# Optimization experiments

Hardware: AMD Instinct MI355X
Metric: run time of the kernel (lower is better)

The kernel has to match this reference:

```python
import jax, jax.numpy as jnp
import numpy as np

NH = 12      # config.n_head
LEVEL = 2    # config.level -> Lmin = 4


def setup_inputs() -> dict:
    key = jax.random.key(0)
    ks = jax.random.split(key, 10)
    B, T, C = 1, 2048, 768
    hs = C // NH
    s = 0.02
    return {
        'x':   jax.random.normal(ks[0], (B, T, C), jnp.float32),
        'Wq':  jax.random.normal(ks[1], (C, C), jnp.float32) * s,
        'Wk':  jax.random.normal(ks[2], (C, C), jnp.float32) * s,
        'Wv':  jax.random.normal(ks[3], (C, C), jnp.float32) * s,
        'Wks': jax.random.normal(ks[4], (hs * hs, hs), jnp.float32) * s,
        'bks': jax.random.normal(ks[5], (hs,), jnp.float32) * s,
        'Wvs': jax.random.normal(ks[6], (hs * hs, hs), jnp.float32) * s,
        'bvs': jax.random.normal(ks[7], (hs,), jnp.float32) * s,
        'Wc':  jax.random.normal(ks[8], (C, C), jnp.float32) * s,
        'bc':  jax.random.normal(ks[9], (C,), jnp.float32) * s,
    }


def reference(x, Wq, Wk, Wv, Wks, bks, Wvs, bvs, Wc, bc):
    B, T, C = x.shape
    hs = C // NH
    Lmin = 2 ** LEVEL
    levelmax = int(np.log2(T))          # T is a power of two -> no ragged tails per level
    scale = hs ** -0.5

    # fla LinearAttention preprocess: bias-free projections + elu feature map (phi = elu+1)
    q = (jax.nn.elu(x @ Wq) + 1.0).reshape(B, T, NH, hs)
    k = (jax.nn.elu(x @ Wk) + 1.0).reshape(B, T, NH, hs)
    v = (x @ Wv).reshape(B, T, NH, hs)

    # per-position linear-attn state increments phi(k) v^T  [B,T,H,hs,hs]
    kv = jnp.einsum('bthi,bthj->bthij', k, v).reshape(B, T, NH, hs * hs)

    # tail features: running state within each block of Lmin (fused_recurrent final states
    # over the ragged per-position tail segments [t - t%Lmin, t])
    tail_feat = jnp.cumsum(kv.reshape(B, T // Lmin, Lmin, NH, hs * hs), axis=2)
    tail_feat = tail_feat.reshape(B, T, NH, hs * hs)

    # hierarchical set features: dyadic block sums at levels LEVEL..levelmax
    cur = kv.reshape(B, T // Lmin, Lmin, NH, hs * hs).sum(axis=2)
    feats, ends = [], []
    for l in range(LEVEL, levelmax + 1):
        n = T // (2 ** l)
        feats.append(cur)
        ends.append(np.arange(1, n + 1) * (2 ** l))   # exclusive end index of each set
        if n >= 2:
            cur = cur.reshape(B, n // 2, 2, NH, hs * hs).sum(axis=2)
    set_feat = jnp.concatenate(feats, axis=1)          # [B, S, H, hs*hs], S = 1023
    ends = np.concatenate(ends)                        # [S]
    mask = ends[None, :] <= (np.arange(T) + 1)[:, None]  # [T, S] causal set mask

    # k_mapping / v_mapping: Linear(hs^2 -> hs)
    K = set_feat @ Wks + bks        # [B,S,H,hs]
    V = set_feat @ Wvs + bvs
    K_tail = tail_feat @ Wks + bks  # [B,T,H,hs]
    V_tail = tail_feat @ Wvs + bvs

    logits = jnp.einsum('bthd,bshd->bhts', q, K) * scale      # [B,H,T,S]
    logits = jnp.where(mask[None, None], logits, jnp.float32(-1e30))
    tail_logit = jnp.einsum('bthd,bthd->bht', q, K_tail) * scale  # [B,H,T]
    att = jax.nn.softmax(jnp.concatenate([logits, tail_logit[..., None]], axis=-1), axis=-1)

    out = jnp.einsum('bhts,bshd->bhtd', att[..., :-1], V)
    out = out + att[..., -1:] * V_tail.transpose(0, 2, 1, 3)  # [B,H,T,hs]
    out = out.transpose(0, 2, 1, 3).reshape(B, T, C)
    return out @ Wc + bc
```

## Files before the change

kernel.cpp:

```cpp
#include <hip/hip_runtime.h>
#include <cstdint>

#define NHEAD 12
#define TLEN 2048
#define CDIM 768
#define NSETS 1023

typedef __attribute__((ext_vector_type(8))) _Float16 half8;
typedef __attribute__((ext_vector_type(2))) __fp16 fp16x2;
typedef __attribute__((ext_vector_type(8))) short short8;
typedef __attribute__((ext_vector_type(4))) float f32x4;

__device__ __forceinline__ float elu1(float x) { return x > 0.f ? x + 1.f : __expf(x); }

__device__ __forceinline__ unsigned pack2_bf16_trunc(float a, float b) {
    unsigned ua = __float_as_uint(a), ub = __float_as_uint(b);
    return __builtin_amdgcn_perm(ub, ua, 0x07060302);
}
__device__ __forceinline__ unsigned pack2_bf16_rne(float a, float b) {
    unsigned ua = __float_as_uint(a), ub = __float_as_uint(b);
    ua = ua + 0x7fff + ((ua >> 16) & 1);
    ub = ub + 0x7fff + ((ub >> 16) & 1);
    return (ub & 0xffff0000u) | (ua >> 16);
}
__device__ __forceinline__ short8 mk_short8(const unsigned* u) {
    union { unsigned w[4]; short8 s; } x;
    x.w[0] = u[0]; x.w[1] = u[1]; x.w[2] = u[2]; x.w[3] = u[3];
    return x.s;
}
__device__ __forceinline__ void split8_bf16(const float* f, short8& hi, short8& lo) {
    unsigned hp[4], lp[4];
    #pragma unroll
    for (int p = 0; p < 4; ++p) {
        float a = f[2 * p], b = f[2 * p + 1];
        unsigned ua = __float_as_uint(a), ub = __float_as_uint(b);
        hp[p] = __builtin_amdgcn_perm(ub, ua, 0x07060302);
        float ra = a - __uint_as_float(ua & 0xffff0000u);
        float rb = b - __uint_as_float(ub & 0xffff0000u);
        lp[p] = pack2_bf16_trunc(ra, rb);
    }
    hi = mk_short8(hp); lo = mk_short8(lp);
}
__device__ __forceinline__ void split8_f16(const float* f, half8& hi, half8& lo) {
    union { fp16x2 h2[4]; half8 h8; } uh, ul;
    #pragma unroll
    for (int jp = 0; jp < 4; ++jp) {
        float a = f[2 * jp], b = f[2 * jp + 1];
        fp16x2 hh = __builtin_amdgcn_cvt_pkrtz(a, b);
        uh.h2[jp] = hh;
        ul.h2[jp] = __builtin_amdgcn_cvt_pkrtz(a - (float)hh[0], b - (float)hh[1]);
    }
    hi = uh.h8; lo = ul.h8;
}

__global__ __launch_bounds__(256) void prep_w768(
    const float* __restrict__ W, _Float16* __restrict__ blob)
{
    const int idx = blockIdx.x * 256 + threadIdx.x;
    const int k = idx / 768, n = idx % 768;
    const int i = k >> 5, kl = k & 31;
    const int quad = kl >> 3, j = kl & 7;
    const int nsg = n >> 4, lane15 = n & 15;
    const int lane = quad * 16 + lane15;
    blob[((size_t)(i * 48 + nsg) * 64 + lane) * 8 + j] = (_Float16)W[idx];
}

__global__ __launch_bounds__(256) void prep_w768x3(
    const float* __restrict__ Wq, const float* __restrict__ Wk,
    const float* __restrict__ Wv, _Float16* __restrict__ blobs)
{
    const int g = blockIdx.x;
    const int sel = g / 2304;
    const float* W = sel == 0 ? Wq : (sel == 1 ? Wk : Wv);
    _Float16* blob = blobs + (size_t)sel * 589824;
    const int idx = (g % 2304) * 256 + threadIdx.x;
    const int k = idx / 768, n = idx % 768;
    const int i = k >> 5, kl = k & 31;
    const int quad = kl >> 3, j = kl & 7;
    const int nsg = n >> 4, lane15 = n & 15;
    const int lane = quad * 16 + lane15;
    blob[((size_t)(i * 48 + nsg) * 64 + lane) * 8 + j] = (_Float16)W[idx];
}

__global__ __launch_bounds__(256) void prep_a_split(
    const float* __restrict__ A, _Float16* __restrict__ hi, _Float16* __restrict__ lo,
    int K)
{
    const int p = blockIdx.x * 256 + threadIdx.x;
    const int lane = p & 63, frag = p >> 6;
    const int k32n = K >> 5;
    const int m16 = frag / k32n, k32 = frag - m16 * k32n;
    const int row = m16 * 16 + (lane & 15);
    const int col = k32 * 32 + (lane >> 4) * 8;
    float f[8];
    *(float4*)&f[0] = *(const float4*)&A[(size_t)row * K + col];
    *(float4*)&f[4] = *(const float4*)&A[(size_t)row * K + col + 4];
    half8 h, l;
    split8_f16(f, h, l);
    *(half8*)&hi[(size_t)p * 8] = h;
    *(half8*)&lo[(size_t)p * 8] = l;
}

template<int QKV>
__global__ __launch_bounds__(256, 3) void gemm_frag(
    const _Float16* __restrict__ Ahi, const _Float16* __restrict__ Alo,
    const _Float16* __restrict__ Bblobs, const float* __restrict__ bias,
    float* __restrict__ outbase)
{
    const int nbx = QKV ? 18 : 6;
    const int cpx = QKV ? 72 : 24;
    int bid = blockIdx.x;
    bid = (bid & 7) * cpx + (bid >> 3);
    const int by  = bid / nbx;
    const int bxg = bid % nbx;
    const int which = QKV ? bxg / 6 : 0;
    const int bxm   = QKV ? bxg % 6 : bxg;
    const half8* __restrict__ Bc = (const half8*)(Bblobs + (size_t)which * 589824);
    float* __restrict__ Cmat = outbase + (size_t)which * ((size_t)TLEN * CDIM);
    const bool act = QKV ? (which < 2) : false;

    const int tid = threadIdx.x;
    const int wave = tid >> 6, lane = tid & 63;
    const int lane15 = lane & 15, quad = lane >> 4;
    const int m16b = by * 4;
    const int nsg0 = bxm * 8 + wave * 2;

    const half8* __restrict__ Ah = (const half8*)Ahi;
    const half8* __restrict__ Al = (const half8*)Alo;

    f32x4 acc[4][2];
    #pragma unroll
    for (int ms = 0; ms < 4; ++ms) {
        acc[ms][0] = (f32x4){0.f, 0.f, 0.f, 0.f};
        acc[ms][1] = (f32x4){0.f, 0.f, 0.f, 0.f};
    }

    const size_t aBase = ((size_t)m16b * 24) * 64 + lane;
    const size_t bBase = (size_t)nsg0 * 64 + lane;

    half8 bb[2], ah[4], al[4];
    bb[0] = Bc[bBase];
    bb[1] = Bc[bBase + 64];
    #pragma unroll
    for (int ms = 0; ms < 4; ++ms) {
        ah[ms] = Ah[aBase + (size_t)ms * (24 * 64)];
        al[ms] = Al[aBase + (size_t)ms * (24 * 64)];
    }

    for (int k32 = 0; k32 < 24; ++k32) {
        half8 bbn[2], ahn[4], aln[4];
        const bool more = (k32 + 1) < 24;
        if (more) {
            const size_t bo = bBase + (size_t)(k32 + 1) * (48 * 64);
            bbn[0] = Bc[bo]; bbn[1] = Bc[bo + 64];
            #pragma unroll
            for (int ms = 0; ms < 4; ++ms) {
                const size_t ao = aBase + (size_t)(k32 + 1) * 64 + (size_t)ms * (24 * 64);
                ahn[ms] = Ah[ao]; aln[ms] = Al[ao];
            }
        }
        #pragma unroll
        for (int ms = 0; ms < 4; ++ms) {
            acc[ms][0] = __builtin_amdgcn_mfma_f32_16x16x32_f16(ah[ms], bb[0], acc[ms][0], 0, 0, 0);
            acc[ms][1] = __builtin_amdgcn_mfma_f32_16x16x32_f16(ah[ms], bb[1], acc[ms][1], 0, 0, 0);
            acc[ms][0] = __builtin_amdgcn_mfma_f32_16x16x32_f16(al[ms], bb[0], acc[ms][0], 0, 0, 0);
            acc[ms][1] = __builtin_amdgcn_mfma_f32_16x16x32_f16(al[ms], bb[1], acc[ms][1], 0, 0, 0);
        }
        if (more) {
            bb[0] = bbn[0]; bb[1] = bbn[1];
            #pragma unroll
            for (int ms = 0; ms < 4; ++ms) { ah[ms] = ahn[ms]; al[ms] = aln[ms]; }
        }
    }

    #pragma unroll
    for (int ms = 0; ms < 4; ++ms)
        #pragma unroll
        for (int nb = 0; nb < 2; ++nb) {
            const int coln = (nsg0 + nb) * 16 + lane15;
            #pragma unroll
            for (int r = 0; r < 4; ++r) {
                const int row = m16b * 16 + ms * 16 + quad * 4 + r;
                float v = acc[ms][nb][r];
                if (!QKV) v += bias[coln];
                if (act) v = elu1(v);
                Cmat[(size_t)row * CDIM + coln] = v;
            }
        }
}

__global__ __launch_bounds__(256) void prep_w(
    const float* __restrict__ Wks, const float* __restrict__ Wvs,
    _Float16* __restrict__ Wblob)
{
    const int idx = blockIdx.x * 256 + threadIdx.x;
    const int kk = idx >> 7, n = idx & 127;
    float f = (n < 64) ? Wks[(size_t)kk * 64 + n] : Wvs[(size_t)kk * 64 + (n - 64)];
    const int i = kk >> 6, kl = kk & 63;
    const int ks = kl >> 5, quad = (kl >> 3) & 3, j = kl & 7;
    const int nsg = n >> 4, lane15 = n & 15;
    const int lane = quad * 16 + lane15;
    const size_t off = ((size_t)(((i * 2 + ks) * 8 + nsg)) * 64 + lane) * 8 + j;
    Wblob[off] = (_Float16)f;
}

__global__ __launch_bounds__(256, 3) void map_f16(
    const float* __restrict__ kbuf, const float* __restrict__ vbuf,
    const _Float16* __restrict__ Wblob,
    float* __restrict__ kkv, float* __restrict__ vvv)
{
    __shared__ float kS[32][68];

    const int tid = threadIdx.x;
    const int p0 = blockIdx.x * 32;
    const int wave = tid >> 6, lane = tid & 63;
    const int lane15 = lane & 15, quad = lane >> 4;

    #pragma unroll
    for (int u = 0; u < 2; ++u) {
        int c = tid + u * 256;
        int row = c >> 4, col = (c & 15) * 4;
        *(float4*)&kS[row][col] = *(const float4*)&kbuf[(size_t)(p0 + row) * 64 + col];
    }

    half8 vrh[2][2];
    #pragma unroll
    for (int mh = 0; mh < 2; ++mh) {
        const size_t pbase = (size_t)(p0 + mh * 16 + lane15) * 64;
        #pragma unroll
        for (int ks = 0; ks < 2; ++ks) {
            float f[8];
            *(float4*)&f[0] = *(const float4*)&vbuf[pbase + ks * 32 + quad * 8];
            *(float4*)&f[4] = *(const float4*)&vbuf[pbase + ks * 32 + quad * 8 + 4];
            union { fp16x2 h2[4]; half8 h8; } u;
            #pragma unroll
            for (int jp = 0; jp < 4; ++jp)
                u.h2[jp] = __builtin_amdgcn_cvt_pkrtz(f[2 * jp], f[2 * jp + 1]);
            vrh[mh][ks] = u.h8;
        }
    }
    __syncthreads();

    const half8* __restrict__ Wc = (const half8*)Wblob;

    f32x4 acc[2][2];
    #pragma unroll
    for (int mh = 0; mh < 2; ++mh)
        #pragma unroll
        for (int nsl = 0; nsl < 2; ++nsl)
            acc[mh][nsl] = (f32x4){0.f, 0.f, 0.f, 0.f};

    half8 b0[2], b1[2], b2[2], b3[2];
    float2 k0, k1, k2, k3;

    auto loadB = [&](half8* b, int s) {
        b[0] = Wc[(size_t)(s * 8 + 2 * wave) * 64 + lane];
        b[1] = Wc[(size_t)(s * 8 + 2 * wave + 1) * 64 + lane];
    };
    auto loadK = [&](float2& kf, int s) {
        kf.x = kS[lane15][s >> 1];
        kf.y = kS[16 + lane15][s >> 1];
    };
    auto compute = [&](const half8* b, float2 kf, int s) {
        const int ks = s & 1;
        #pragma unroll
        for (int mh = 0; mh < 2; ++mh) {
            float kv = mh ? kf.y : kf.x;
            fp16x2 k2v = __builtin_amdgcn_cvt_pkrtz(kv, kv);
            union { fp16x2 h2[4]; half8 h8; } kb;
            kb.h2[0] = k2v; kb.h2[1] = k2v; kb.h2[2] = k2v; kb.h2[3] = k2v;
            half8 a = kb.h8 * vrh[mh][ks];
            acc[mh][0] = __builtin_amdgcn_mfma_f32_16x16x32_f16(a, b[0], acc[mh][0], 0, 0, 0);
            acc[mh][1] = __builtin_amdgcn_mfma_f32_16x16x32_f16(a, b[1], acc[mh][1], 0, 0, 0);
        }
    };

    loadB(b0, 0); loadB(b1, 1); loadB(b2, 2); loadB(b3, 3);
    loadK(k0, 0); loadK(k1, 1); loadK(k2, 2); loadK(k3, 3);
    for (int s = 0; s < 128; s += 4) {
        const bool more = (s + 4) < 128;
        compute(b0, k0, s);
        compute(b1, k1, s + 1);
        if (more) { loadB(b0, s + 4); loadK(k0, s + 4); loadB(b1, s + 5); loadK(k1, s + 5); }
        compute(b2, k2, s + 2);
        compute(b3, k3, s + 3);
        if (more) { loadB(b2, s + 6); loadK(k2, s + 6); loadB(b3, s + 7); loadK(k3, s + 7); }
    }

    #pragma unroll
    for (int mh = 0; mh < 2; ++mh)
        #pragma unroll
        for (int nsl = 0; nsl < 2; ++nsl) {
            int n128 = (2 * wave + nsl) * 16 + lane15;
            float* dst = (n128 < 64) ? kkv : vvv;
            int col = n128 & 63;
            #pragma unroll
            for (int r = 0; r < 4; ++r) {
                int p = p0 + mh * 16 + quad * 4 + r;
                dst[(size_t)p * 64 + col] = acc[mh][nsl][r];
            }
        }
}

__global__ __launch_bounds__(256) void set_lower(
    const float* __restrict__ kkv, const float* __restrict__ vvv,
    const float* __restrict__ bks, const float* __restrict__ bvs,
    float* __restrict__ Kset, float* __restrict__ Vset,
    float* __restrict__ scrK, float* __restrict__ scrV,
    float* __restrict__ Kt, float* __restrict__ Vt)
{
    __shared__ float curK[63][64];
    __shared__ float curV[63][64];
    const int tid = threadIdx.x;
    const int col = tid & 63, grp = tid >> 6;
    const int h = blockIdx.x % NHEAD;
    const int c = blockIdx.x / NHEAD;
    const int t0 = c * 128;
    const float bk = bks[col], bv = bvs[col];

    for (int j = grp; j < 32; j += 4) {
        const size_t rbase = (size_t)(t0 + j * 4) * CDIM + h * 64 + col;
        const float* pk = kkv + rbase;
        const float* pv = vvv + rbase;
        float* ptK = Kt + rbase;
        float* ptV = Vt + rbase;
        float sk = bk, sv = bv;
        #pragma unroll
        for (int u = 0; u < 4; ++u) {
            sk += pk[(size_t)u * CDIM];
            sv += pv[(size_t)u * CDIM];
            ptK[(size_t)u * CDIM] = sk;
            ptV[(size_t)u * CDIM] = sv;
        }
        curK[j][col] = sk - bk; curV[j][col] = sv - bv;
        size_t o = ((size_t)(c * 32 + j) * NHEAD + h) * 64 + col;
        Kset[o] = sk; Vset[o] = sv;
    }
    __syncthreads();

    const int LBASE[6] = {0, 32, 48, 56, 60, 62};
    const int GBASE[6] = {0, 512, 768, 896, 960, 992};
    #pragma unroll
    for (int li = 1; li < 6; ++li) {
        const int ns = 32 >> li;
        for (int j = grp; j < ns; j += 4) {
            float sk = curK[LBASE[li - 1] + 2 * j][col] + curK[LBASE[li - 1] + 2 * j + 1][col];
            float sv = curV[LBASE[li - 1] + 2 * j][col] + curV[LBASE[li - 1] + 2 * j + 1][col];
            curK[LBASE[li] + j][col] = sk; curV[LBASE[li] + j][col] = sv;
            size_t o = ((size_t)(GBASE[li] + c * ns + j) * NHEAD + h) * 64 + col;
            Kset[o] = sk + bk; Vset[o] = sv + bv;
        }
        __syncthreads();
    }

    if (grp == 0) {
        scrK[((size_t)h * 16 + c) * 64 + col] = curK[62][col];
        scrV[((size_t)h * 16 + c) * 64 + col] = curV[62][col];
    }
}

__global__ __launch_bounds__(256) void set_upper(
    const float* __restrict__ scrK, const float* __restrict__ scrV,
    const float* __restrict__ bks, const float* __restrict__ bvs,
    float* __restrict__ Kset, float* __restrict__ Vset)
{
    __shared__ float cK[15][64], cV[15][64];
    const int h = blockIdx.x;
    const int tid = threadIdx.x, col = tid & 63, grp = tid >> 6;
    const float bk = bks[col], bv = bvs[col];

    for (int j = grp; j < 8; j += 4) {
        float sk = scrK[((size_t)h * 16 + 2 * j) * 64 + col] + scrK[((size_t)h * 16 + 2 * j + 1) * 64 + col];
        float sv = scrV[((size_t)h * 16 + 2 * j) * 64 + col] + scrV[((size_t)h * 16 + 2 * j + 1) * 64 + col];
        cK[j][col] = sk; cV[j][col] = sv;
        size_t o = ((size_t)(1008 + j) * NHEAD + h) * 64 + col;
        Kset[o] = sk + bk; Vset[o] = sv + bv;
    }
    __syncthreads();
    const int LB[4] = {0, 8, 12, 14};
    const int GB[4] = {1008, 1016, 1020, 1022};
    #pragma unroll
    for (int li = 1; li < 4; ++li) {
        const int ns = 8 >> li;
        for (int j = grp; j < ns; j += 4) {
            float sk = cK[LB[li - 1] + 2 * j][col] + cK[LB[li - 1] + 2 * j + 1][col];
            float sv = cV[LB[li - 1] + 2 * j][col] + cV[LB[li - 1] + 2 * j + 1][col];
            cK[LB[li] + j][col] = sk; cV[LB[li] + j][col] = sv;
            size_t o = ((size_t)(GB[li] + j) * NHEAD + h) * 64 + col;
            Kset[o] = sk + bk; Vset[o] = sv + bv;
        }
        __syncthreads();
    }
}

__global__ __launch_bounds__(256, 3) void attn_mfma(
    const float* __restrict__ qbuf, const float* __restrict__ Kset,
    const float* __restrict__ Vset, const float* __restrict__ Ktail,
    const float* __restrict__ Vtail, float* __restrict__ attout)
{
    __shared__ int   sidAll[1024], sendAll[1024];
    __shared__ float sS[32][68];
    __shared__ unsigned sP[32][40];
    __shared__ unsigned vP[64][40];
    __shared__ float arowS[32];
    __shared__ float alS[32], ptS[32];

    const int tid = threadIdx.x;
    const int b   = 63 - (blockIdx.x / NHEAD);
    const int h   = blockIdx.x % NHEAD;
    const int T0  = b * 32;
    const int wave = tid >> 6, lane = tid & 63;
    const int lane15 = lane & 15, quad = lane >> 4;

    const int Tend = T0 + 32;
    const int LOFF[10] = {0, 512, 768, 896, 960, 992, 1008, 1016, 1020, 1022};
    int pfx[10], Vtot = 0;
    #pragma unroll
    for (int li = 0; li < 10; ++li) { pfx[li] = Vtot; Vtot += Tend >> (li + 2); }
    const int ntiles = (Vtot + 63) >> 6;

    for (int j = tid; j < 1024; j += 256) {
        int s_ = 0, e_ = 0x7fffffff;
        if (j < Vtot) {
            int li = 0;
            #pragma unroll
            for (int u = 1; u < 10; ++u) if (j >= pfx[u]) li = u;
            int idx = j - pfx[li];
            s_ = LOFF[li] + idx;
            e_ = (idx + 1) << (li + 2);
        }
        sidAll[j] = s_; sendAll[j] = e_;
    }

    short8 Qhi[2][2], Qlo[2][2];
    #pragma unroll
    for (int ms = 0; ms < 2; ++ms)
        #pragma unroll
        for (int kt = 0; kt < 2; ++kt) {
            const float* qp = qbuf + ((size_t)(T0 + ms * 16 + lane15) * NHEAD + h) * 64 + kt * 32 + quad * 8;
            float f[8];
            *(float4*)&f[0] = *(const float4*)qp;
            *(float4*)&f[4] = *(const float4*)(qp + 4);
            split8_bf16(f, Qhi[ms][kt], Qlo[ms][kt]);
        }

    __syncthreads();

    const int row = tid >> 3, part = tid & 7;
    float mreg = -1e30f, lreg = 0.f;

    f32x4 oacc[2];
    oacc[0] = (f32x4){0.f, 0.f, 0.f, 0.f};
    oacc[1] = (f32x4){0.f, 0.f, 0.f, 0.f};

    float4 Vr[4];
    float4 Kr[4];
    const int sp = tid >> 3, dd = (tid & 7) * 8;
    auto prefV = [&](int tile) {
        int sa = sidAll[tile * 64 + 2 * sp];
        int sb = sidAll[tile * 64 + 2 * sp + 1];
        const float* pa = Vset + ((size_t)sa * NHEAD + h) * 64 + dd;
        const float* pb = Vset + ((size_t)sb * NHEAD + h) * 64 + dd;
        Vr[0] = *(const float4*)pa; Vr[1] = *(const float4*)(pa + 4);
        Vr[2] = *(const float4*)pb; Vr[3] = *(const float4*)(pb + 4);
    };
    auto prefK = [&](int tile) {
        int sK = sidAll[tile * 64 + wave * 16 + lane15];
        const float* kp = Kset + ((size_t)sK * NHEAD + h) * 64 + quad * 8;
        Kr[0] = *(const float4*)kp;        Kr[1] = *(const float4*)(kp + 4);
        Kr[2] = *(const float4*)(kp + 32); Kr[3] = *(const float4*)(kp + 36);
    };
    prefV(0); prefK(0);

    for (int tile = 0; tile < ntiles; ++tile) {
        __syncthreads();

        {
            const float* va = (const float*)&Vr[0];
            const float* vb = (const float*)&Vr[2];
            #pragma unroll
            for (int i = 0; i < 8; ++i)
                vP[dd + i][sp] = pack2_bf16_rne(va[i], vb[i]);
        }

        short8 Khi[2], Klo[2];
        {
            float f[8];
            *(float4*)&f[0] = Kr[0]; *(float4*)&f[4] = Kr[1];
            split8_bf16(f, Khi[0], Klo[0]);
            *(float4*)&f[0] = Kr[2]; *(float4*)&f[4] = Kr[3];
            split8_bf16(f, Khi[1], Klo[1]);
        }

        f32x4 lacc[2];
        lacc[0] = (f32x4){0.f, 0.f, 0.f, 0.f};
        lacc[1] = (f32x4){0.f, 0.f, 0.f, 0.f};
        #pragma unroll
        for (int kt = 0; kt < 2; ++kt)
            #pragma unroll
            for (int ms = 0; ms < 2; ++ms) {
                lacc[ms] = __builtin_amdgcn_mfma_f32_16x16x32_bf16(Qhi[ms][kt], Khi[kt], lacc[ms], 0, 0, 0);
                lacc[ms] = __builtin_amdgcn_mfma_f32_16x16x32_bf16(Qlo[ms][kt], Khi[kt], lacc[ms], 0, 0, 0);
                lacc[ms] = __builtin_amdgcn_mfma_f32_16x16x32_bf16(Qhi[ms][kt], Klo[kt], lacc[ms], 0, 0, 0);
            }

        {
            const int sendv = sendAll[tile * 64 + wave * 16 + lane15];
            #pragma unroll
            for (int ms = 0; ms < 2; ++ms)
                #pragma unroll
                for (int r = 0; r < 4; ++r) {
                    int qrow = ms * 16 + quad * 4 + r;
                    bool ok = (T0 + qrow + 1) >= sendv;
                    sS[qrow][wave * 16 + lane15] = ok ? lacc[ms][r] * 0.125f : -1e30f;
                }
        }

        if (tile + 1 < ntiles) { prefV(tile + 1); prefK(tile + 1); }

        __syncthreads();

        {
            float4 a = *(float4*)&sS[row][part * 8];
            float4 c4 = *(float4*)&sS[row][part * 8 + 4];
            float mx = fmaxf(fmaxf(fmaxf(a.x, a.y), fmaxf(a.z, a.w)),
                             fmaxf(fmaxf(c4.x, c4.y), fmaxf(c4.z, c4.w)));
            mx = fmaxf(mx, __shfl_xor(mx, 1));
            mx = fmaxf(mx, __shfl_xor(mx, 2));
            mx = fmaxf(mx, __shfl_xor(mx, 4));
            float mnew = fmaxf(mreg, mx);
            float al = __expf(mreg - mnew);
            mreg = mnew;
            a.x = a.x > -1e29f ? __expf(a.x - mnew) : 0.f;
            a.y = a.y > -1e29f ? __expf(a.y - mnew) : 0.f;
            a.z = a.z > -1e29f ? __expf(a.z - mnew) : 0.f;
            a.w = a.w > -1e29f ? __expf(a.w - mnew) : 0.f;
            c4.x = c4.x > -1e29f ? __expf(c4.x - mnew) : 0.f;
            c4.y = c4.y > -1e29f ? __expf(c4.y - mnew) : 0.f;
            c4.z = c4.z > -1e29f ? __expf(c4.z - mnew) : 0.f;
            c4.w = c4.w > -1e29f ? __expf(c4.w - mnew) : 0.f;
            float sm = (a.x + a.y + a.z + a.w) + (c4.x + c4.y + c4.z + c4.w);
            sm += __shfl_xor(sm, 1);
            sm += __shfl_xor(sm, 2);
            sm += __shfl_xor(sm, 4);
            lreg = al * lreg + sm;
            unsigned w0 = pack2_bf16_rne(a.x, a.y);
            unsigned w1 = pack2_bf16_rne(a.z, a.w);
            unsigned w2 = pack2_bf16_rne(c4.x, c4.y);
            unsigned w3 = pack2_bf16_rne(c4.z, c4.w);
            *(uint4*)&sP[row][part * 4] = make_uint4(w0, w1, w2, w3);
            if (part == 0) arowS[row] = al;
        }

        __syncthreads();

        #pragma unroll
        for (int ms = 0; ms < 2; ++ms)
            #pragma unroll
            for (int r = 0; r < 4; ++r)
                oacc[ms][r] *= arowS[ms * 16 + quad * 4 + r];

        #pragma unroll
        for (int kt = 0; kt < 2; ++kt) {
            short8 Vf = *(short8*)&vP[wave * 16 + lane15][kt * 16 + quad * 4];
            #pragma unroll
            for (int ms = 0; ms < 2; ++ms) {
                short8 Pf = *(short8*)&sP[ms * 16 + lane15][kt * 16 + quad * 4];
                oacc[ms] = __builtin_amdgcn_mfma_f32_16x16x32_bf16(Pf, Vf, oacc[ms], 0, 0, 0);
            }
        }
    }

    {
        const float* qr = qbuf  + ((size_t)(T0 + row) * NHEAD + h) * 64 + part * 8;
        const float* kr = Ktail + ((size_t)(T0 + row) * NHEAD + h) * 64 + part * 8;
        float4 qa = *(const float4*)qr, qb = *(const float4*)(qr + 4);
        float4 ka = *(const float4*)kr, kb = *(const float4*)(kr + 4);
        float dp = qa.x * ka.x + qa.y * ka.y + qa.z * ka.z + qa.w * ka.w
                 + qb.x * kb.x + qb.y * kb.y + qb.z * kb.z + qb.w * kb.w;
        dp += __shfl_xor(dp, 1);
        dp += __shfl_xor(dp, 2);
        dp += __shfl_xor(dp, 4);
        float tl = dp * 0.125f;
        float mf = fmaxf(mreg, tl);
        float al = __expf(mreg - mf);
        float pt = __expf(tl - mf);
        float lf = al * lreg + pt;
        float inv = 1.f / lf;
        if (part == 0) { alS[row] = al * inv; ptS[row] = pt * inv; }
    }
    __syncthreads();

    #pragma unroll
    for (int ms = 0; ms < 2; ++ms)
        #pragma unroll
        for (int r = 0; r < 4; ++r) {
            int qrow = ms * 16 + quad * 4 + r;
            int col = wave * 16 + lane15;
            float al_inv = alS[qrow];
            float ptinv = ptS[qrow];
            size_t base = ((size_t)(T0 + qrow) * NHEAD + h) * 64 + col;
            attout[base] = oacc[ms][r] * al_inv + ptinv * Vtail[base];
        }
}

extern "C" void kernel_launch(void* const* d_in, const int* in_sizes, int n_in,
                              void* d_out, int out_size, void* d_ws, size_t ws_size,
                              hipStream_t stream)
{
    const float* x   = (const float*)d_in[0];
    const float* Wq  = (const float*)d_in[1];
    const float* Wk  = (const float*)d_in[2];
    const float* Wv  = (const float*)d_in[3];
    const float* Wks = (const float*)d_in[4];
    const float* bks = (const float*)d_in[5];
    const float* Wvs = (const float*)d_in[6];
    const float* bvs = (const float*)d_in[7];
    const float* Wc  = (const float*)d_in[8];
    const float* bc  = (const float*)d_in[9];
    float* out = (float*)d_out;

    float* ws = (float*)d_ws;
    const size_t TC = (size_t)TLEN * CDIM;
    float* q      = ws;
    float* k      = q + TC;
    float* v      = k + TC;
    float* kkv    = v + TC;
    float* vvv    = kkv + TC;
    float* Kt     = vvv + TC;
    float* Vt     = Kt + TC;
    float* Kset   = Vt + TC;
    float* Vset   = Kset + (size_t)NSETS * CDIM;
    float* attout = Vset + (size_t)NSETS * CDIM;
    _Float16* WblobMap = (_Float16*)attout;
    _Float16* blobQKV  = (_Float16*)(attout + 262144);
    float* scrK = attout + 1146880;
    float* scrV = scrK + 12 * 16 * 64;
    _Float16* blobC = (_Float16*)k;
    _Float16* xhi = (_Float16*)kkv;
    _Float16* xlo = xhi + TC;
    _Float16* atthi = (_Float16*)Kt;
    _Float16* attlo = atthi + TC;

    prep_w768x3<<<3 * 2304, 256, 0, stream>>>(Wq, Wk, Wv, blobQKV);
    prep_w<<<(4096 * 128) / 256, 256, 0, stream>>>(Wks, Wvs, WblobMap);

    prep_a_split<<<(TLEN * CDIM / 8) / 256, 256, 0, stream>>>(x, xhi, xlo, CDIM);
    gemm_frag<1><<<576, 256, 0, stream>>>(xhi, xlo, blobQKV, nullptr, q);

    map_f16<<<(TLEN * NHEAD) / 32, 256, 0, stream>>>(k, v, WblobMap, kkv, vvv);

    prep_w768<<<2304, 256, 0, stream>>>(Wc, blobC);

    set_lower<<<16 * NHEAD, 256, 0, stream>>>(kkv, vvv, bks, bvs, Kset, Vset, scrK, scrV, Kt, Vt);
    set_upper<<<NHEAD, 256, 0, stream>>>(scrK, scrV, bks, bvs, Kset, Vset);

    attn_mfma<<<(TLEN / 32) * NHEAD, 256, 0, stream>>>(q, Kset, Vset, Kt, Vt, attout);

    prep_a_split<<<(TLEN * CDIM / 8) / 256, 256, 0, stream>>>(attout, atthi, attlo, CDIM);
    gemm_frag<0><<<192, 256, 0, stream>>>(atthi, attlo, blobC, bc, out);
}
```

Measured before the change: 221.9 us.

## Split map_f16 reduction over two blocks and pre-pack k as fp16 in LDS

The K=4096 reduction in map_f16 is split in half across two blocks, doubling the grid and raising the occupancy hint. Each half writes a partial result to its own buffer, and set_lower sums the two partials as it reads them. The k values are converted to packed fp16 once when staged into shared memory, which removes the per-iteration conversion. The cost is extra global traffic for the second pair of partial buffers, plus the risk that attout-adjacent workspace is reused while still live.

```diff
diff --git a/kernel.cpp b/kernel.cpp
--- a/kernel.cpp
+++ b/kernel.cpp
@@ -204,23 +204,32 @@
     Wblob[off] = (_Float16)f;
 }
 
-__global__ __launch_bounds__(256, 3) void map_f16(
+__global__ __launch_bounds__(256, 6) void map_f16(
     const float* __restrict__ kbuf, const float* __restrict__ vbuf,
     const _Float16* __restrict__ Wblob,
-    float* __restrict__ kkv, float* __restrict__ vvv)
-{
-    __shared__ float kS[32][68];
+    float* __restrict__ kkvA, float* __restrict__ vvvA,
+    float* __restrict__ kkvB, float* __restrict__ vvvB)
+{
+    __shared__ unsigned kU[32][36];
 
     const int tid = threadIdx.x;
-    const int p0 = blockIdx.x * 32;
+    const int pg = blockIdx.x >> 1, sh = blockIdx.x & 1;
+    const int p0 = pg * 32;
     const int wave = tid >> 6, lane = tid & 63;
     const int lane15 = lane & 15, quad = lane >> 4;
 
-    #pragma unroll
-    for (int u = 0; u < 2; ++u) {
-        int c = tid + u * 256;
-        int row = c >> 4, col = (c & 15) * 4;
-        *(float4*)&kS[row][col] = *(const float4*)&kbuf[(size_t)(p0 + row) * 64 + col];
+    {
+        const int row = tid >> 3, ib = (tid & 7) * 4;
+        float4 k4 = *(const float4*)&kbuf[(size_t)(p0 + row) * 64 + sh * 32 + ib];
+        union { fp16x2 h; unsigned u; } c0, c1, c2, c3;
+        c0.h = __builtin_amdgcn_cvt_pkrtz(k4.x, k4.x);
+        c1.h = __builtin_amdgcn_cvt_pkrtz(k4.y, k4.y);
+        c2.h = __builtin_amdgcn_cvt_pkrtz(k4.z, k4.z);
+        c3.h = __builtin_amdgcn_cvt_pkrtz(k4.w, k4.w);
+        kU[row][ib + 0] = c0.u;
+        kU[row][ib + 1] = c1.u;
+        kU[row][ib + 2] = c2.u;
+        kU[row][ib + 3] = c3.u;
     }
 
     half8 vrh[2][2];
@@ -251,24 +260,24 @@
             acc[mh][nsl] = (f32x4){0.f, 0.f, 0.f, 0.f};
 
     half8 b0[2], b1[2], b2[2], b3[2];
-    float2 k0, k1, k2, k3;
-
-    auto loadB = [&](half8* b, int s) {
+    unsigned k0x, k0y, k1x, k1y, k2x, k2y, k3x, k3y;
+
+    auto loadB = [&](half8* b, int sl) {
+        const int s = sh * 64 + sl;
         b[0] = Wc[(size_t)(s * 8 + 2 * wave) * 64 + lane];
         b[1] = Wc[(size_t)(s * 8 + 2 * wave + 1) * 64 + lane];
     };
-    auto loadK = [&](float2& kf, int s) {
-        kf.x = kS[lane15][s >> 1];
-        kf.y = kS[16 + lane15][s >> 1];
+    auto loadK = [&](unsigned& kx, unsigned& ky, int sl) {
+        kx = kU[lane15][sl >> 1];
+        ky = kU[16 + lane15][sl >> 1];
     };
-    auto compute = [&](const half8* b, float2 kf, int s) {
-        const int ks = s & 1;
+    auto compute = [&](const half8* b, unsigned kx, unsigned ky, int sl) {
+        const int ks = sl & 1;
         #pragma unroll
         for (int mh = 0; mh < 2; ++mh) {
-            float kv = mh ? kf.y : kf.x;
-            fp16x2 k2v = __builtin_amdgcn_cvt_pkrtz(kv, kv);
-            union { fp16x2 h2[4]; half8 h8; } kb;
-            kb.h2[0] = k2v; kb.h2[1] = k2v; kb.h2[2] = k2v; kb.h2[3] = k2v;
+            union { unsigned w[4]; half8 h8; } kb;
+            unsigned u = mh ? ky : kx;
+            kb.w[0] = u; kb.w[1] = u; kb.w[2] = u; kb.w[3] = u;
             half8 a = kb.h8 * vrh[mh][ks];
             acc[mh][0] = __builtin_amdgcn_mfma_f32_16x16x32_f16(a, b[0], acc[mh][0], 0, 0, 0);
             acc[mh][1] = __builtin_amdgcn_mfma_f32_16x16x32_f16(a, b[1], acc[mh][1], 0, 0, 0);
@@ -276,17 +285,19 @@
     };
 
     loadB(b0, 0); loadB(b1, 1); loadB(b2, 2); loadB(b3, 3);
-    loadK(k0, 0); loadK(k1, 1); loadK(k2, 2); loadK(k3, 3);
-    for (int s = 0; s < 128; s += 4) {
-        const bool more = (s + 4) < 128;
-        compute(b0, k0, s);
-        compute(b1, k1, s + 1);
-        if (more) { loadB(b0, s + 4); loadK(k0, s + 4); loadB(b1, s + 5); loadK(k1, s + 5); }
-        compute(b2, k2, s + 2);
-        compute(b3, k3, s + 3);
-        if (more) { loadB(b2, s + 6); loadK(k2, s + 6); loadB(b3, s + 7); loadK(k3, s + 7); }
-    }
-
+    loadK(k0x, k0y, 0); loadK(k1x, k1y, 1); loadK(k2x, k2y, 2); loadK(k3x, k3y, 3);
+    for (int sl = 0; sl < 64; sl += 4) {
+        const bool more = (sl + 4) < 64;
+        compute(b0, k0x, k0y, sl);
+        compute(b1, k1x, k1y, sl + 1);
+        if (more) { loadB(b0, sl + 4); loadK(k0x, k0y, sl + 4); loadB(b1, sl + 5); loadK(k1x, k1y, sl + 5); }
+        compute(b2, k2x, k2y, sl + 2);
+        compute(b3, k3x, k3y, sl + 3);
+        if (more) { loadB(b2, sl + 6); loadK(k2x, k2y, sl + 6); loadB(b3, sl + 7); loadK(k3x, k3y, sl + 7); }
+    }
+
+    float* __restrict__ kkv = sh ? kkvB : kkvA;
+    float* __restrict__ vvv = sh ? vvvB : vvvA;
     #pragma unroll
     for (int mh = 0; mh < 2; ++mh)
         #pragma unroll
@@ -303,7 +314,8 @@
 }
 
 __global__ __launch_bounds__(256) void set_lower(
-    const float* __restrict__ kkv, const float* __restrict__ vvv,
+    const float* __restrict__ kkvA, const float* __restrict__ vvvA,
+    const float* __restrict__ kkvB, const float* __restrict__ vvvB,
     const float* __restrict__ bks, const float* __restrict__ bvs,
     float* __restrict__ Kset, float* __restrict__ Vset,
     float* __restrict__ scrK, float* __restrict__ scrV,
@@ -320,15 +332,17 @@
 
     for (int j = grp; j < 32; j += 4) {
         const size_t rbase = (size_t)(t0 + j * 4) * CDIM + h * 64 + col;
-        const float* pk = kkv + rbase;
-        const float* pv = vvv + rbase;
+        const float* pkA = kkvA + rbase;
+        const float* pvA = vvvA + rbase;
+        const float* pkB = kkvB + rbase;
+        const float* pvB = vvvB + rbase;
         float* ptK = Kt + rbase;
         float* ptV = Vt + rbase;
         float sk = bk, sv = bv;
         #pragma unroll
         for (int u = 0; u < 4; ++u) {
-            sk += pk[(size_t)u * CDIM];
-            sv += pv[(size_t)u * CDIM];
+            sk += pkA[(size_t)u * CDIM] + pkB[(size_t)u * CDIM];
+            sv += pvA[(size_t)u * CDIM] + pvB[(size_t)u * CDIM];
             ptK[(size_t)u * CDIM] = sk;
             ptV[(size_t)u * CDIM] = sv;
         }
@@ -636,6 +650,8 @@
     _Float16* blobQKV  = (_Float16*)(attout + 262144);
     float* scrK = attout + 1146880;
     float* scrV = scrK + 12 * 16 * 64;
+    float* kkvB = attout + TC;
+    float* vvvB = kkvB + TC;
     _Float16* blobC = (_Float16*)k;
     _Float16* xhi = (_Float16*)kkv;
     _Float16* xlo = xhi + TC;
@@ -648,11 +664,11 @@
     prep_a_split<<<(TLEN * CDIM / 8) / 256, 256, 0, stream>>>(x, xhi, xlo, CDIM);
     gemm_frag<1><<<576, 256, 0, stream>>>(xhi, xlo, blobQKV, nullptr, q);
 
-    map_f16<<<(TLEN * NHEAD) / 32, 256, 0, stream>>>(k, v, WblobMap, kkv, vvv);
+    map_f16<<<(TLEN * NHEAD / 32) * 2, 256, 0, stream>>>(k, v, WblobMap, kkv, vvv, kkvB, vvvB);
 
     prep_w768<<<2304, 256, 0, stream>>>(Wc, blobC);
 
-    set_lower<<<16 * NHEAD, 256, 0, stream>>>(kkv, vvv, bks, bvs, Kset, Vset, scrK, scrV, Kt, Vt);
+    set_lower<<<16 * NHEAD, 256, 0, stream>>>(kkv, vvv, kkvB, vvvB, bks, bvs, Kset, Vset, scrK, scrV, Kt, Vt);
     set_upper<<<NHEAD, 256, 0, stream>>>(scrK, scrV, bks, bvs, Kset, Vset);
 
     attn_mfma<<<(TLEN / 32) * NHEAD, 256, 0, stream>>>(q, Kset, Vset, Kt, Vt, attout);
```

New measurement: 225.7 us. No clear change (+1.7%).

## Fuse attention output split into attn kernel, merge Wc prep, enlarge map tiles

Applied to the files above, without the earlier changes.

The attention kernel now stages its output tile in shared memory and writes the fp16 hi/lo fragment layout directly. This removes the separate prep_a_split pass over the attention output and its fp32 round trip through global memory. The Wc weight conversion is folded into the batched QKV weight-prep launch, which drops one kernel launch. map_f16 now processes 64 positions per block with k pre-converted to packed fp16 in shared memory, reusing each B-fragment load across more rows. The cost is higher register use in map_f16, so occupancy drops to 2 blocks per CU, and workspace aliasing changes.

```diff
diff --git a/kernel.cpp b/kernel.cpp
--- a/kernel.cpp
+++ b/kernel.cpp
@@ -53,26 +53,15 @@
     hi = uh.h8; lo = ul.h8;
 }
 
-__global__ __launch_bounds__(256) void prep_w768(
-    const float* __restrict__ W, _Float16* __restrict__ blob)
-{
-    const int idx = blockIdx.x * 256 + threadIdx.x;
-    const int k = idx / 768, n = idx % 768;
-    const int i = k >> 5, kl = k & 31;
-    const int quad = kl >> 3, j = kl & 7;
-    const int nsg = n >> 4, lane15 = n & 15;
-    const int lane = quad * 16 + lane15;
-    blob[((size_t)(i * 48 + nsg) * 64 + lane) * 8 + j] = (_Float16)W[idx];
-}
-
-__global__ __launch_bounds__(256) void prep_w768x3(
+__global__ __launch_bounds__(256) void prep_w768x4(
     const float* __restrict__ Wq, const float* __restrict__ Wk,
-    const float* __restrict__ Wv, _Float16* __restrict__ blobs)
+    const float* __restrict__ Wv, const float* __restrict__ Wc4,
+    _Float16* __restrict__ blobQKV, _Float16* __restrict__ blobC)
 {
     const int g = blockIdx.x;
     const int sel = g / 2304;
-    const float* W = sel == 0 ? Wq : (sel == 1 ? Wk : Wv);
-    _Float16* blob = blobs + (size_t)sel * 589824;
+    const float* W = sel == 0 ? Wq : (sel == 1 ? Wk : (sel == 2 ? Wv : Wc4));
+    _Float16* blob = (sel < 3) ? (blobQKV + (size_t)sel * 589824) : blobC;
     const int idx = (g % 2304) * 256 + threadIdx.x;
     const int k = idx / 768, n = idx % 768;
     const int i = k >> 5, kl = k & 31;
@@ -204,28 +193,36 @@
     Wblob[off] = (_Float16)f;
 }
 
-__global__ __launch_bounds__(256, 3) void map_f16(
+__global__ __launch_bounds__(256, 2) void map_f16(
     const float* __restrict__ kbuf, const float* __restrict__ vbuf,
     const _Float16* __restrict__ Wblob,
     float* __restrict__ kkv, float* __restrict__ vvv)
 {
-    __shared__ float kS[32][68];
+    __shared__ unsigned kU[64][65];
 
     const int tid = threadIdx.x;
-    const int p0 = blockIdx.x * 32;
+    const int p0 = blockIdx.x * 64;
     const int wave = tid >> 6, lane = tid & 63;
     const int lane15 = lane & 15, quad = lane >> 4;
 
-    #pragma unroll
-    for (int u = 0; u < 2; ++u) {
-        int c = tid + u * 256;
-        int row = c >> 4, col = (c & 15) * 4;
-        *(float4*)&kS[row][col] = *(const float4*)&kbuf[(size_t)(p0 + row) * 64 + col];
-    }
-
-    half8 vrh[2][2];
-    #pragma unroll
-    for (int mh = 0; mh < 2; ++mh) {
+    {
+        const int row = tid >> 2, cb = (tid & 3) * 16;
+        float f[16];
+        *(float4*)&f[0]  = *(const float4*)&kbuf[(size_t)(p0 + row) * 64 + cb + 0];
+        *(float4*)&f[4]  = *(const float4*)&kbuf[(size_t)(p0 + row) * 64 + cb + 4];
+        *(float4*)&f[8]  = *(const float4*)&kbuf[(size_t)(p0 + row) * 64 + cb + 8];
+        *(float4*)&f[12] = *(const float4*)&kbuf[(size_t)(p0 + row) * 64 + cb + 12];
+        #pragma unroll
+        for (int i = 0; i < 16; ++i) {
+            union { fp16x2 h; unsigned u; } c;
+            c.h = __builtin_amdgcn_cvt_pkrtz(f[i], f[i]);
+            kU[row][cb + i] = c.u;
+        }
+    }
+
+    half8 vrh[4][2];
+    #pragma unroll
+    for (int mh = 0; mh < 4; ++mh) {
         const size_t pbase = (size_t)(p0 + mh * 16 + lane15) * 64;
         #pragma unroll
         for (int ks = 0; ks < 2; ++ks) {
@@ -243,52 +240,53 @@
 
     const half8* __restrict__ Wc = (const half8*)Wblob;
 
-    f32x4 acc[2][2];
-    #pragma unroll
-    for (int mh = 0; mh < 2; ++mh)
+    f32x4 acc[4][2];
+    #pragma unroll
+    for (int mh = 0; mh < 4; ++mh)
         #pragma unroll
         for (int nsl = 0; nsl < 2; ++nsl)
             acc[mh][nsl] = (f32x4){0.f, 0.f, 0.f, 0.f};
 
     half8 b0[2], b1[2], b2[2], b3[2];
-    float2 k0, k1, k2, k3;
+    unsigned ka0[4], ka1[4], ka2[4], ka3[4];
 
     auto loadB = [&](half8* b, int s) {
         b[0] = Wc[(size_t)(s * 8 + 2 * wave) * 64 + lane];
         b[1] = Wc[(size_t)(s * 8 + 2 * wave + 1) * 64 + lane];
     };
-    auto loadK = [&](float2& kf, int s) {
-        kf.x = kS[lane15][s >> 1];
-        kf.y = kS[16 + lane15][s >> 1];
+    auto loadK = [&](unsigned* ka, int s) {
+        const int i = s >> 1;
+        #pragma unroll
+        for (int mh = 0; mh < 4; ++mh) ka[mh] = kU[mh * 16 + lane15][i];
     };
-    auto compute = [&](const half8* b, float2 kf, int s) {
+    auto compute = [&](const half8* b, const unsigned* ka, int s) {
         const int ks = s & 1;
         #pragma unroll
-        for (int mh = 0; mh < 2; ++mh) {
-            float kv = mh ? kf.y : kf.x;
-            fp16x2 k2v = __builtin_amdgcn_cvt_pkrtz(kv, kv);
-            union { fp16x2 h2[4]; half8 h8; } kb;
-            kb.h2[0] = k2v; kb.h2[1] = k2v; kb.h2[2] = k2v; kb.h2[3] = k2v;
-            half8 a = kb.h8 * vrh[mh][ks];
-            acc[mh][0] = __builtin_amdgcn_mfma_f32_16x16x32_f16(a, b[0], acc[mh][0], 0, 0, 0);
-            acc[mh][1] = __builtin_amdgcn_mfma_f32_16x16x32_f16(a, b[1], acc[mh][1], 0, 0, 0);
+        for (int mh = 0; mh < 4; ++mh) {
+            union { unsigned u; fp16x2 h; } ku; ku.u = ka[mh];
+            union { fp16x2 h2[4]; half8 h8; } va, ra;
+            va.h8 = vrh[mh][ks];
+            #pragma unroll
+            for (int jp = 0; jp < 4; ++jp) ra.h2[jp] = ku.h * va.h2[jp];
+            acc[mh][0] = __builtin_amdgcn_mfma_f32_16x16x32_f16(ra.h8, b[0], acc[mh][0], 0, 0, 0);
+            acc[mh][1] = __builtin_amdgcn_mfma_f32_16x16x32_f16(ra.h8, b[1], acc[mh][1], 0, 0, 0);
         }
     };
 
     loadB(b0, 0); loadB(b1, 1); loadB(b2, 2); loadB(b3, 3);
-    loadK(k0, 0); loadK(k1, 1); loadK(k2, 2); loadK(k3, 3);
+    loadK(ka0, 0); loadK(ka1, 1); loadK(ka2, 2); loadK(ka3, 3);
     for (int s = 0; s < 128; s += 4) {
         const bool more = (s + 4) < 128;
-        compute(b0, k0, s);
-        compute(b1, k1, s + 1);
-        if (more) { loadB(b0, s + 4); loadK(k0, s + 4); loadB(b1, s + 5); loadK(k1, s + 5); }
-        compute(b2, k2, s + 2);
-        compute(b3, k3, s + 3);
-        if (more) { loadB(b2, s + 6); loadK(k2, s + 6); loadB(b3, s + 7); loadK(k3, s + 7); }
-    }
-
-    #pragma unroll
-    for (int mh = 0; mh < 2; ++mh)
+        compute(b0, ka0, s);
+        compute(b1, ka1, s + 1);
+        if (more) { loadB(b0, s + 4); loadK(ka0, s + 4); loadB(b1, s + 5); loadK(ka1, s + 5); }
+        compute(b2, ka2, s + 2);
+        compute(b3, ka3, s + 3);
+        if (more) { loadB(b2, s + 6); loadK(ka2, s + 6); loadB(b3, s + 7); loadK(ka3, s + 7); }
+    }
+
+    #pragma unroll
+    for (int mh = 0; mh < 4; ++mh)
         #pragma unroll
         for (int nsl = 0; nsl < 2; ++nsl) {
             int n128 = (2 * wave + nsl) * 16 + lane15;
@@ -396,7 +394,8 @@
 __global__ __launch_bounds__(256, 3) void attn_mfma(
     const float* __restrict__ qbuf, const float* __restrict__ Kset,
     const float* __restrict__ Vset, const float* __restrict__ Ktail,
-    const float* __restrict__ Vtail, float* __restrict__ attout)
+    const float* __restrict__ Vtail,
+    _Float16* __restrict__ atthi, _Float16* __restrict__ attlo)
 {
     __shared__ int   sidAll[1024], sendAll[1024];
     __shared__ float sS[32][68];
@@ -597,11 +596,22 @@
         for (int r = 0; r < 4; ++r) {
             int qrow = ms * 16 + quad * 4 + r;
             int col = wave * 16 + lane15;
-            float al_inv = alS[qrow];
-            float ptinv = ptS[qrow];
             size_t base = ((size_t)(T0 + qrow) * NHEAD + h) * 64 + col;
-            attout[base] = oacc[ms][r] * al_inv + ptinv * Vtail[base];
-        }
+            sS[qrow][col] = oacc[ms][r] * alS[qrow] + ptS[qrow] * Vtail[base];
+        }
+    __syncthreads();
+
+    {
+        const int kt = wave >> 1, msf = wave & 1;
+        float f[8];
+        *(float4*)&f[0] = *(const float4*)&sS[msf * 16 + lane15][kt * 32 + quad * 8];
+        *(float4*)&f[4] = *(const float4*)&sS[msf * 16 + lane15][kt * 32 + quad * 8 + 4];
+        half8 hh, ll;
+        split8_f16(f, hh, ll);
+        const size_t frag = (size_t)(b * 2 + msf) * 24 + (2 * h + kt);
+        *(half8*)&atthi[(frag * 64 + lane) * 8] = hh;
+        *(half8*)&attlo[(frag * 64 + lane) * 8] = ll;
+    }
 }
 
 extern "C" void kernel_launch(void* const* d_in, const int* in_sizes, int n_in,
@@ -636,27 +646,24 @@
     _Float16* blobQKV  = (_Float16*)(attout + 262144);
     float* scrK = attout + 1146880;
     float* scrV = scrK + 12 * 16 * 64;
-    _Float16* blobC = (_Float16*)k;
+    _Float16* blobC = (_Float16*)(attout + 1171456);
     _Float16* xhi = (_Float16*)kkv;
     _Float16* xlo = xhi + TC;
-    _Float16* atthi = (_Float16*)Kt;
+    _Float16* atthi = (_Float16*)vvv;
     _Float16* attlo = atthi + TC;
 
-    prep_w768x3<<<3 * 2304, 256, 0, stream>>>(Wq, Wk, Wv, blobQKV);
+    prep_w768x4<<<4 * 2304, 256, 0, stream>>>(Wq, Wk, Wv, Wc, blobQKV, blobC);
     prep_w<<<(4096 * 128) / 256, 256, 0, stream>>>(Wks, Wvs, WblobMap);
 
     prep_a_split<<<(TLEN * CDIM / 8) / 256, 256, 0, stream>>>(x, xhi, xlo, CDIM);
     gemm_frag<1><<<576, 256, 0, stream>>>(xhi, xlo, blobQKV, nullptr, q);
 
-    map_f16<<<(TLEN * NHEAD) / 32, 256, 0, stream>>>(k, v, WblobMap, kkv, vvv);
-
-    prep_w768<<<2304, 256, 0, stream>>>(Wc, blobC);
+    map_f16<<<(TLEN * NHEAD) / 64, 256, 0, stream>>>(k, v, WblobMap, kkv, vvv);
 
     set_lower<<<16 * NHEAD, 256, 0, stream>>>(kkv, vvv, bks, bvs, Kset, Vset, scrK, scrV, Kt, Vt);
     set_upper<<<NHEAD, 256, 0, stream>>>(scrK, scrV, bks, bvs, Kset, Vset);
 
-    attn_mfma<<<(TLEN / 32) * NHEAD, 256, 0, stream>>>(q, Kset, Vset, Kt, Vt, attout);
-
-    prep_a_split<<<(TLEN * CDIM / 8) / 256, 256, 0, stream>>>(attout, atthi, attlo, CDIM);
+    attn_mfma<<<(TLEN / 32) * NHEAD, 256, 0, stream>>>(q, Kset, Vset, Kt, Vt, atthi, attlo);
+
     gemm_frag<0><<<192, 256, 0, stream>>>(atthi, attlo, blobC, bc, out);
 }
```

Result: faster. 209.3 us (-5.7%).
